# Kernel optimization log

Measured on AMD Instinct MI355X. Metric: run time of the kernel, lower is better.

## Reference

```python
import jax, jax.numpy as jnp
import numpy as np

N_SCALES = 128
F_MIN, F_MAX = 20.0, 450.0
FS = 2000
SIGMA = 6.0
HOP = 64


def make_morlet_filters():
    """Replicates CWTTransform.__init__ filter-bank construction."""
    freqs = np.logspace(np.log10(F_MIN), np.log10(F_MAX), N_SCALES)
    filters_real, filters_imag = [], []
    max_len = 0
    for f in freqs:
        scale = SIGMA / (2 * np.pi * f)
        t_half = int(4 * scale * FS)
        t = np.arange(-t_half, t_half + 1) / FS
        gaussian = np.exp(-t ** 2 / (2 * scale ** 2))
        w_real = gaussian * np.cos(2 * np.pi * f * t)
        w_imag = gaussian * np.sin(2 * np.pi * f * t)
        norm = np.sqrt(np.sum(w_real ** 2 + w_imag ** 2))
        filters_real.append(w_real / norm)
        filters_imag.append(w_imag / norm)
        max_len = max(max_len, len(w_real))
    if max_len % 2 == 0:
        max_len += 1
    weight_real = np.zeros((N_SCALES, 1, max_len), dtype=np.float32)
    weight_imag = np.zeros((N_SCALES, 1, max_len), dtype=np.float32)
    for i, (wr, wi) in enumerate(zip(filters_real, filters_imag)):
        pad_l = (max_len - len(wr)) // 2
        pad_r = max_len - len(wr) - pad_l
        weight_real[i, 0] = np.pad(wr, (pad_l, pad_r))
        weight_imag[i, 0] = np.pad(wi, (pad_l, pad_r))
    return jnp.asarray(weight_real), jnp.asarray(weight_imag)


def setup_inputs() -> dict:
    key = jax.random.key(0)
    B, C, T = 4, 3, 16384
    x = jax.random.normal(key, (B, C, T), dtype=jnp.float32)
    weight_real, weight_imag = make_morlet_filters()
    return {"x": x, "weight_real": weight_real, "weight_imag": weight_imag,
            "hop_length": HOP}


def reference(x, weight_real, weight_imag, hop_length):
    B, C, T = x.shape
    K = weight_real.shape[-1]          # filter length (763, odd)
    pad = K // 2
    # Fold channels into the batch dim: each channel convolved independently
    # with the same 1-in / n_scales-out filter bank (as the per-channel loop).
    sig = x.reshape(B * C, 1, T)
    sig = jnp.pad(sig, ((0, 0), (0, 0), (pad, pad)), mode="reflect")

    def conv(w):
        return jax.lax.conv_general_dilated(
            sig, w, window_strides=(1,), padding="VALID",
            dimension_numbers=("NCH", "OIH", "NCH"))  # -> [B*C, n_scales, T]

    real = conv(weight_real)
    imag = conv(weight_imag)
    mag = jnp.log1p(jnp.sqrt(real * real + imag * imag + 1e-8))
    if hop_length > 1:
        L = mag.shape[-1]
        n_frames = L // hop_length
        mag = mag[..., : n_frames * hop_length]
        mag = mag.reshape(B * C, mag.shape[1], n_frames, hop_length).mean(-1)
    return mag.reshape(B, C, mag.shape[1], mag.shape[-1])
```

## Files before the change

### kernel.cpp

```cpp
#include <hip/hip_runtime.h>
#include <hip/hip_bf16.h>
#include <math.h>


#define T_LEN 16384
#define KW    763
#define HALF  381
#define NSC   128
#define NFR   256
#define TPB   256
#define TBLK  128
#define NSLOT 119
#define WLEN  (8 * NSLOT)
#define CP_SH (NSLOT * 8)
#define KSTR  4096
#define IOFF  106496

typedef __attribute__((ext_vector_type(8))) short short8;
typedef __attribute__((ext_vector_type(4))) float f32x4;

union S8U { short8 s; unsigned u[4]; };

static __device__ inline unsigned cvt_pk_bf16(float lo, float hi) {
    unsigned r;
    asm volatile("v_cvt_pk_bf16_f32 %0, %1, %2" : "=v"(r) : "v"(lo), "v"(hi));
    return r;
}

static __device__ inline short8 ld8g(const unsigned short* p) {
    short8 r;
    __builtin_memcpy(&r, p, 16);
    return r;
}

#define MFMA16(A, B, C) __builtin_amdgcn_mfma_f32_16x16x32_bf16(A, B, C, 0, 0, 0)

__global__ __launch_bounds__(256) void pack_weights(
    const float* __restrict__ wr, const float* __restrict__ wi,
    unsigned short* __restrict__ a2)
{
    const int i = blockIdx.x * 256 + threadIdx.x;
    const int pad1 = 26 * 128 * 4;
    if (i >= 2 * pad1) return;
    short8 pk;
    const int plane = i / pad1;
    const int r0    = i - plane * pad1;
    const int kc32  = r0 >> 9;
    if (kc32 < 24) {
        const int row   = (r0 >> 2) & 127;
        const int oct   = r0 & 3;
        const int kbase = kc32 * 32 + oct * 8;
        const float* w = plane ? wi : wr;
        unsigned short v[8];
        #pragma unroll
        for (int j = 0; j < 8; ++j) {
            const int k = kbase + j;
            float f = (k < KW) ? w[row * KW + k] : 0.f;
            __hip_bfloat16 b = __float2bfloat16(f);
            v[j] = *(unsigned short*)&b;
        }
        __builtin_memcpy(&pk, v, 16);
    } else {
        #pragma unroll
        for (int j = 0; j < 8; ++j) ((unsigned short*)&pk)[j] = 0;
    }
    *(short8*)(a2 + (size_t)i * 8) = pk;
}

__global__ __launch_bounds__(TPB, 3) void cwt_mfma_kernel(
    const float* __restrict__ x,
    const unsigned short* __restrict__ a2,
    float* __restrict__ out)
{
    __shared__ __align__(16) float xw[WLEN];
    __shared__ __align__(16) short cps[8 * CP_SH];

    const int tid  = threadIdx.x;
    const int lane = tid & 63;
    const int ws   = tid >> 6;
    const int n    = lane & 15;
    const int oct  = lane >> 4;
    const int blk  = blockIdx.x;
    const int sg   = blockIdx.y;
    const int t0   = blk * TBLK;
    const int wse  = (ws + blk) & 3;

    const float* xsig = x + sg * T_LEN;
    for (int u = tid; u < WLEN; u += TPB) {
        int gg = t0 - HALF + u;
        if (gg < 0) gg = -gg;
        if (gg >= T_LEN) gg = 2 * T_LEN - 2 - gg;
        xw[u] = xsig[gg];
    }
    __syncthreads();

    for (int u = tid; u < 8 * NSLOT; u += TPB) {
        const int m = u >> 3;
        const int c = (u + m) & 7;
        const int base = 8 * m + c;
        S8U pk;
        pk.u[0] = cvt_pk_bf16(xw[base],     xw[base + 1]);
        pk.u[1] = cvt_pk_bf16(xw[base + 2], xw[base + 3]);
        pk.u[2] = cvt_pk_bf16(xw[base + 4], xw[base + 5]);
        pk.u[3] = cvt_pk_bf16(xw[base + 6], xw[base + 7]);
        *(short8*)&cps[c * CP_SH + m * 8] = pk.s;
    }
    __syncthreads();

    const float lg20  = 1.301029995663981f;
    const float stepl = (2.653212513775344f - 1.301029995663981f) / 127.0f;

    const int ng   = (wse == 0) ? 1 : (wse == 3) ? 3 : 2;
    const int gseq = (wse == 0) ? 0x0 : (wse == 1) ? 0x71 :
                     (wse == 2) ? 0x32 : 0x654;

    for (int gi = 0; gi < ng; ++gi) {
        const int g  = (gseq >> (4 * gi)) & 15;
        const int s0 = 16 * g;
        float fg = exp10f(lg20 + (float)s0 * stepl);
        int hg = (int)(7639.43726841098f / fg) + 2;
        if (hg > HALF) hg = HALF;
        const int k0 = (HALF - hg) & ~31;
        const int ks = (HALF + hg + 1 - k0 + 31) >> 5;

        f32x4 acR0, acI0, acR1, acI1, acR2, acI2, acR3, acI3;
        f32x4 acR4, acI4, acR5, acI5, acR6, acI6, acR7, acI7;
        acR0 = acI0 = acR1 = acI1 = (f32x4){0.f, 0.f, 0.f, 0.f};
        acR2 = acI2 = acR3 = acI3 = (f32x4){0.f, 0.f, 0.f, 0.f};
        acR4 = acI4 = acR5 = acI5 = (f32x4){0.f, 0.f, 0.f, 0.f};
        acR6 = acI6 = acR7 = acI7 = (f32x4){0.f, 0.f, 0.f, 0.f};

        const unsigned short* pA = a2 + (size_t)(k0 >> 5) * KSTR
                                      + ((s0 + n) * 4 + oct) * 8;
        short8 aAr = ld8g(pA),            aAi = ld8g(pA + IOFF);
        short8 aBr = ld8g(pA + KSTR),     aBi = ld8g(pA + KSTR + IOFF);
        short8 aCr, aCi, aDr, aDi;

        const int s_i0 = n + 8 * oct + k0;
        const char* bp = (const char*)cps
                       + (s_i0 & 7) * (2 * CP_SH)
                       + ((s_i0 >> 3) << 4);
        short8 b0 = *(const short8*)(bp);
        short8 b1 = *(const short8*)(bp + 32);
        short8 b2 = *(const short8*)(bp + 64);
        short8 b3 = *(const short8*)(bp + 96);
        short8 b4 = *(const short8*)(bp + 128);
        short8 b5 = *(const short8*)(bp + 160);
        short8 b6 = *(const short8*)(bp + 192);
        short8 b7 = *(const short8*)(bp + 224);

#define KSTEP(AR, AI, PR, PI, PFO, S0_,S1_,S2_,S3_,S4_,S5_,S6_,S7_, R0, R1)  \
        {                                                                     \
            __builtin_amdgcn_s_setprio(1);                                    \
            acR0 = MFMA16(AR, S0_, acR0);  acI0 = MFMA16(AI, S0_, acI0);      \
            acR1 = MFMA16(AR, S1_, acR1);  acI1 = MFMA16(AI, S1_, acI1);      \
            S0_ = *(const short8*)(bp + (R0));                                \
            S1_ = *(const short8*)(bp + (R1));                                \
            PR = ld8g(pA + (PFO));  PI = ld8g(pA + (PFO) + IOFF);             \
            acR2 = MFMA16(AR, S2_, acR2);  acI2 = MFMA16(AI, S2_, acI2);      \
            acR3 = MFMA16(AR, S3_, acR3);  acI3 = MFMA16(AI, S3_, acI3);      \
            acR4 = MFMA16(AR, S4_, acR4);  acI4 = MFMA16(AI, S4_, acI4);      \
            acR5 = MFMA16(AR, S5_, acR5);  acI5 = MFMA16(AI, S5_, acI5);      \
            acR6 = MFMA16(AR, S6_, acR6);  acI6 = MFMA16(AI, S6_, acI6);      \
            acR7 = MFMA16(AR, S7_, acR7);  acI7 = MFMA16(AI, S7_, acI7);      \
            __builtin_amdgcn_s_setprio(0);                                    \
        }

#define KSTEP_NR(AR, AI, S0_,S1_,S2_,S3_,S4_,S5_,S6_,S7_)                     \
        {                                                                     \
            __builtin_amdgcn_s_setprio(1);                                    \
            acR0 = MFMA16(AR, S0_, acR0);  acI0 = MFMA16(AI, S0_, acI0);      \
            acR1 = MFMA16(AR, S1_, acR1);  acI1 = MFMA16(AI, S1_, acI1);      \
            acR2 = MFMA16(AR, S2_, acR2);  acI2 = MFMA16(AI, S2_, acI2);      \
            acR3 = MFMA16(AR, S3_, acR3);  acI3 = MFMA16(AI, S3_, acI3);      \
            acR4 = MFMA16(AR, S4_, acR4);  acI4 = MFMA16(AI, S4_, acI4);      \
            acR5 = MFMA16(AR, S5_, acR5);  acI5 = MFMA16(AI, S5_, acI5);      \
            acR6 = MFMA16(AR, S6_, acR6);  acI6 = MFMA16(AI, S6_, acI6);      \
            acR7 = MFMA16(AR, S7_, acR7);  acI7 = MFMA16(AI, S7_, acI7);      \
            __builtin_amdgcn_s_setprio(0);                                    \
        }

        for (int it = 0; it + 4 <= ks; it += 4) {
            KSTEP(aAr, aAi, aCr, aCi, 2 * KSTR,
                  b0, b1, b2, b3, b4, b5, b6, b7, 256, 288)
            KSTEP(aBr, aBi, aDr, aDi, 3 * KSTR,
                  b2, b3, b4, b5, b6, b7, b0, b1, 320, 352)
            KSTEP(aCr, aCi, aAr, aAi, 4 * KSTR,
                  b4, b5, b6, b7, b0, b1, b2, b3, 384, 416)
            KSTEP(aDr, aDi, aBr, aBi, 5 * KSTR,
                  b6, b7, b0, b1, b2, b3, b4, b5, 448, 480)
            pA += 4 * KSTR;
            bp += 256;
        }
        if (ks & 2) {
            KSTEP(aAr, aAi, aCr, aCi, 2 * KSTR,
                  b0, b1, b2, b3, b4, b5, b6, b7, 256, 288)
            KSTEP_NR(aBr, aBi, b2, b3, b4, b5, b6, b7, b0, b1)
        }
#undef KSTEP
#undef KSTEP_NR

        const float C = 0.6931471805599453f / 64.0f;
        #pragma unroll
        for (int f = 0; f < 2; ++f) {
            float v[4];
            #pragma unroll
            for (int r = 0; r < 4; ++r) {
                float s;
                if (f == 0) {
                    float m0 = fmaf(acR0[r], acR0[r], fmaf(acI0[r], acI0[r], 1e-8f));
                    float m1 = fmaf(acR1[r], acR1[r], fmaf(acI1[r], acI1[r], 1e-8f));
                    float m2 = fmaf(acR2[r], acR2[r], fmaf(acI2[r], acI2[r], 1e-8f));
                    float m3 = fmaf(acR3[r], acR3[r], fmaf(acI3[r], acI3[r], 1e-8f));
                    s = __builtin_amdgcn_logf(1.f + __builtin_amdgcn_sqrtf(m0))
                      + __builtin_amdgcn_logf(1.f + __builtin_amdgcn_sqrtf(m1))
                      + __builtin_amdgcn_logf(1.f + __builtin_amdgcn_sqrtf(m2))
                      + __builtin_amdgcn_logf(1.f + __builtin_amdgcn_sqrtf(m3));
                } else {
                    float m0 = fmaf(acR4[r], acR4[r], fmaf(acI4[r], acI4[r], 1e-8f));
                    float m1 = fmaf(acR5[r], acR5[r], fmaf(acI5[r], acI5[r], 1e-8f));
                    float m2 = fmaf(acR6[r], acR6[r], fmaf(acI6[r], acI6[r], 1e-8f));
                    float m3 = fmaf(acR7[r], acR7[r], fmaf(acI7[r], acI7[r], 1e-8f));
                    s = __builtin_amdgcn_logf(1.f + __builtin_amdgcn_sqrtf(m0))
                      + __builtin_amdgcn_logf(1.f + __builtin_amdgcn_sqrtf(m1))
                      + __builtin_amdgcn_logf(1.f + __builtin_amdgcn_sqrtf(m2))
                      + __builtin_amdgcn_logf(1.f + __builtin_amdgcn_sqrtf(m3));
                }
                v[r] = s;
            }
            #pragma unroll
            for (int r = 0; r < 4; ++r) v[r] += __shfl_xor(v[r], 1);
            float w0 = (lane & 1) ? v[1] : v[0];
            float w1 = (lane & 1) ? v[3] : v[2];
            w0 += __shfl_xor(w0, 2);
            w1 += __shfl_xor(w1, 2);
            float u = (lane & 2) ? w1 : w0;
            u += __shfl_xor(u, 4);
            u += __shfl_xor(u, 8);
            if (n < 4) {
                const int srow  = s0 + 4 * oct + (n & 3);
                const int frame = blk * 2 + f;
                out[(sg * NSC + srow) * NFR + frame] = u * C;
            }
        }
    }
}

extern "C" void kernel_launch(void* const* d_in, const int* in_sizes, int n_in,
                              void* d_out, int out_size, void* d_ws, size_t ws_size,
                              hipStream_t stream) {
    const float* x  = (const float*)d_in[0];
    const float* wr = (const float*)d_in[1];
    const float* wi = (const float*)d_in[2];
    float* out = (float*)d_out;
    unsigned short* a2 = (unsigned short*)d_ws;

    pack_weights<<<104, 256, 0, stream>>>(wr, wi, a2);
    dim3 grid(T_LEN / TBLK, 12);
    cwt_mfma_kernel<<<grid, TPB, 0, stream>>>(x, a2, out);
}
```

Before: 38.90 us.

## Fuse weight bf16 packing into CWT kernel, load fp32 filters directly

Removes the separate pack_weights launch and instead loads fp32 filter rows straight from the input arrays, converting to bf16 in registers with v_cvt_pk_bf16 right before each MFMA. It also adds a special tail path for the longest-filter group (g==0) that zeroes the elements past the 763-tap end, so the row-contiguous layout does not read into the next row. This saves one kernel launch and its global round trip. In exchange, every block now does uncoalesced, double-width fp32 weight loads plus conversion work inside the hot loop.

```diff
diff --git a/kernel.cpp b/kernel.cpp
--- a/kernel.cpp
+++ b/kernel.cpp
@@ -13,8 +13,6 @@
 #define NSLOT 119
 #define WLEN  (8 * NSLOT)
 #define CP_SH (NSLOT * 8)
-#define KSTR  4096
-#define IOFF  106496
 
 typedef __attribute__((ext_vector_type(8))) short short8;
 typedef __attribute__((ext_vector_type(4))) float f32x4;
@@ -27,49 +25,35 @@
     return r;
 }
 
-static __device__ inline short8 ld8g(const unsigned short* p) {
-    short8 r;
-    __builtin_memcpy(&r, p, 16);
-    return r;
+static __device__ inline short8 ld8w(const float* p) {
+    float f[8];
+    __builtin_memcpy(f, p, 32);
+    S8U pk;
+    pk.u[0] = cvt_pk_bf16(f[0], f[1]);
+    pk.u[1] = cvt_pk_bf16(f[2], f[3]);
+    pk.u[2] = cvt_pk_bf16(f[4], f[5]);
+    pk.u[3] = cvt_pk_bf16(f[6], f[7]);
+    return pk.s;
+}
+
+static __device__ inline short8 ld8w_tail(const float* p, int oct) {
+    float f[8];
+    __builtin_memcpy(f, p, 32);
+    if (oct == 3) { f[3] = 0.f; f[4] = 0.f; f[5] = 0.f; f[6] = 0.f; f[7] = 0.f; }
+    S8U pk;
+    pk.u[0] = cvt_pk_bf16(f[0], f[1]);
+    pk.u[1] = cvt_pk_bf16(f[2], f[3]);
+    pk.u[2] = cvt_pk_bf16(f[4], f[5]);
+    pk.u[3] = cvt_pk_bf16(f[6], f[7]);
+    return pk.s;
 }
 
 #define MFMA16(A, B, C) __builtin_amdgcn_mfma_f32_16x16x32_bf16(A, B, C, 0, 0, 0)
-
-__global__ __launch_bounds__(256) void pack_weights(
-    const float* __restrict__ wr, const float* __restrict__ wi,
-    unsigned short* __restrict__ a2)
-{
-    const int i = blockIdx.x * 256 + threadIdx.x;
-    const int pad1 = 26 * 128 * 4;
-    if (i >= 2 * pad1) return;
-    short8 pk;
-    const int plane = i / pad1;
-    const int r0    = i - plane * pad1;
-    const int kc32  = r0 >> 9;
-    if (kc32 < 24) {
-        const int row   = (r0 >> 2) & 127;
-        const int oct   = r0 & 3;
-        const int kbase = kc32 * 32 + oct * 8;
-        const float* w = plane ? wi : wr;
-        unsigned short v[8];
-        #pragma unroll
-        for (int j = 0; j < 8; ++j) {
-            const int k = kbase + j;
-            float f = (k < KW) ? w[row * KW + k] : 0.f;
-            __hip_bfloat16 b = __float2bfloat16(f);
-            v[j] = *(unsigned short*)&b;
-        }
-        __builtin_memcpy(&pk, v, 16);
-    } else {
-        #pragma unroll
-        for (int j = 0; j < 8; ++j) ((unsigned short*)&pk)[j] = 0;
-    }
-    *(short8*)(a2 + (size_t)i * 8) = pk;
-}
 
 __global__ __launch_bounds__(TPB, 3) void cwt_mfma_kernel(
     const float* __restrict__ x,
-    const unsigned short* __restrict__ a2,
+    const float* __restrict__ wr,
+    const float* __restrict__ wi,
     float* __restrict__ out)
 {
     __shared__ __align__(16) float xw[WLEN];
@@ -130,10 +114,10 @@
         acR4 = acI4 = acR5 = acI5 = (f32x4){0.f, 0.f, 0.f, 0.f};
         acR6 = acI6 = acR7 = acI7 = (f32x4){0.f, 0.f, 0.f, 0.f};
 
-        const unsigned short* pA = a2 + (size_t)(k0 >> 5) * KSTR
-                                      + ((s0 + n) * 4 + oct) * 8;
-        short8 aAr = ld8g(pA),            aAi = ld8g(pA + IOFF);
-        short8 aBr = ld8g(pA + KSTR),     aBi = ld8g(pA + KSTR + IOFF);
+        const float* pR = wr + (size_t)(s0 + n) * KW + k0 + oct * 8;
+        const float* pI = wi + (size_t)(s0 + n) * KW + k0 + oct * 8;
+        short8 aAr = ld8w(pR),      aAi = ld8w(pI);
+        short8 aBr = ld8w(pR + 32), aBi = ld8w(pI + 32);
         short8 aCr, aCi, aDr, aDi;
 
         const int s_i0 = n + 8 * oct + k0;
@@ -149,14 +133,14 @@
         short8 b6 = *(const short8*)(bp + 192);
         short8 b7 = *(const short8*)(bp + 224);
 
-#define KSTEP(AR, AI, PR, PI, PFO, S0_,S1_,S2_,S3_,S4_,S5_,S6_,S7_, R0, R1)  \
+#define KSTEP(AR, AI, PR_, PI_, PFO, S0_,S1_,S2_,S3_,S4_,S5_,S6_,S7_, R0, R1) \
         {                                                                     \
             __builtin_amdgcn_s_setprio(1);                                    \
             acR0 = MFMA16(AR, S0_, acR0);  acI0 = MFMA16(AI, S0_, acI0);      \
             acR1 = MFMA16(AR, S1_, acR1);  acI1 = MFMA16(AI, S1_, acI1);      \
             S0_ = *(const short8*)(bp + (R0));                                \
             S1_ = *(const short8*)(bp + (R1));                                \
-            PR = ld8g(pA + (PFO));  PI = ld8g(pA + (PFO) + IOFF);             \
+            PR_ = ld8w(pR + (PFO));  PI_ = ld8w(pI + (PFO));                  \
             acR2 = MFMA16(AR, S2_, acR2);  acI2 = MFMA16(AI, S2_, acI2);      \
             acR3 = MFMA16(AR, S3_, acR3);  acI3 = MFMA16(AI, S3_, acI3);      \
             acR4 = MFMA16(AR, S4_, acR4);  acI4 = MFMA16(AI, S4_, acI4);      \
@@ -180,20 +164,43 @@
             __builtin_amdgcn_s_setprio(0);                                    \
         }
 
-        for (int it = 0; it + 4 <= ks; it += 4) {
-            KSTEP(aAr, aAi, aCr, aCi, 2 * KSTR,
+        const int itEnd = (g == 0) ? 20 : ks;
+
+        for (int it = 0; it + 4 <= itEnd; it += 4) {
+            KSTEP(aAr, aAi, aCr, aCi, 64,
                   b0, b1, b2, b3, b4, b5, b6, b7, 256, 288)
-            KSTEP(aBr, aBi, aDr, aDi, 3 * KSTR,
+            KSTEP(aBr, aBi, aDr, aDi, 96,
                   b2, b3, b4, b5, b6, b7, b0, b1, 320, 352)
-            KSTEP(aCr, aCi, aAr, aAi, 4 * KSTR,
+            KSTEP(aCr, aCi, aAr, aAi, 128,
                   b4, b5, b6, b7, b0, b1, b2, b3, 384, 416)
-            KSTEP(aDr, aDi, aBr, aBi, 5 * KSTR,
+            KSTEP(aDr, aDi, aBr, aBi, 160,
                   b6, b7, b0, b1, b2, b3, b4, b5, 448, 480)
-            pA += 4 * KSTR;
+            pR += 128;  pI += 128;
             bp += 256;
         }
-        if (ks & 2) {
-            KSTEP(aAr, aAi, aCr, aCi, 2 * KSTR,
+        if (g == 0) {
+            KSTEP(aAr, aAi, aCr, aCi, 64,
+                  b0, b1, b2, b3, b4, b5, b6, b7, 256, 288)
+            {
+                __builtin_amdgcn_s_setprio(1);
+                acR0 = MFMA16(aBr, b2, acR0);  acI0 = MFMA16(aBi, b2, acI0);
+                acR1 = MFMA16(aBr, b3, acR1);  acI1 = MFMA16(aBi, b3, acI1);
+                b2 = *(const short8*)(bp + 320);
+                b3 = *(const short8*)(bp + 352);
+                aDr = ld8w_tail(pR + 96, oct);  aDi = ld8w_tail(pI + 96, oct);
+                acR2 = MFMA16(aBr, b4, acR2);  acI2 = MFMA16(aBi, b4, acI2);
+                acR3 = MFMA16(aBr, b5, acR3);  acI3 = MFMA16(aBi, b5, acI3);
+                acR4 = MFMA16(aBr, b6, acR4);  acI4 = MFMA16(aBi, b6, acI4);
+                acR5 = MFMA16(aBr, b7, acR5);  acI5 = MFMA16(aBi, b7, acI5);
+                acR6 = MFMA16(aBr, b0, acR6);  acI6 = MFMA16(aBi, b0, acI6);
+                acR7 = MFMA16(aBr, b1, acR7);  acI7 = MFMA16(aBi, b1, acI7);
+                __builtin_amdgcn_s_setprio(0);
+            }
+            KSTEP(aCr, aCi, aAr, aAi, 128,
+                  b4, b5, b6, b7, b0, b1, b2, b3, 384, 416)
+            KSTEP_NR(aDr, aDi, b6, b7, b0, b1, b2, b3, b4, b5)
+        } else if (ks & 2) {
+            KSTEP(aAr, aAi, aCr, aCi, 64,
                   b0, b1, b2, b3, b4, b5, b6, b7, 256, 288)
             KSTEP_NR(aBr, aBi, b2, b3, b4, b5, b6, b7, b0, b1)
         }
@@ -249,13 +256,12 @@
 extern "C" void kernel_launch(void* const* d_in, const int* in_sizes, int n_in,
                               void* d_out, int out_size, void* d_ws, size_t ws_size,
                               hipStream_t stream) {
+    (void)in_sizes; (void)n_in; (void)out_size; (void)d_ws; (void)ws_size;
     const float* x  = (const float*)d_in[0];
     const float* wr = (const float*)d_in[1];
     const float* wi = (const float*)d_in[2];
     float* out = (float*)d_out;
-    unsigned short* a2 = (unsigned short*)d_ws;
-
-    pack_weights<<<104, 256, 0, stream>>>(wr, wi, a2);
+
     dim3 grid(T_LEN / TBLK, 12);
-    cwt_mfma_kernel<<<grid, TPB, 0, stream>>>(x, a2, out);
-}
+    cwt_mfma_kernel<<<grid, TPB, 0, stream>>>(x, wr, wi, out);
+}
```

After: 51.43 us. +32.2%, slower.
